# Kernel tuning notes

Hardware: AMD Instinct MI355X
Metric: run time of the kernel (lower is better)

The kernel has to match this reference:

```python
import jax, jax.numpy as jnp
import numpy as np

B, T, C, H = 4, 2048, 1024, 16
D = C // H  # head dim = 64


def setup_inputs() -> dict:
    key = jax.random.key(0)
    ks = jax.random.split(key, 5)
    s = 1.0 / np.sqrt(C)
    return {
        "x": jax.random.normal(ks[0], (B, T, C), dtype=jnp.float32),
        "Wq": jax.random.normal(ks[1], (C, C), dtype=jnp.float32) * s,
        "bq": jnp.zeros((C,), dtype=jnp.float32),
        "Wk": jax.random.normal(ks[2], (C, C), dtype=jnp.float32) * s,
        "bk": jnp.zeros((C,), dtype=jnp.float32),
        "Wv": jax.random.normal(ks[3], (C, C), dtype=jnp.float32) * s,
        "bv": jnp.zeros((C,), dtype=jnp.float32),
        "Wp": jax.random.normal(ks[4], (C, C), dtype=jnp.float32) * s,
        "bp": jnp.zeros((C,), dtype=jnp.float32),
    }


def reference(x, Wq, bq, Wk, bk, Wv, bv, Wp, bp):
    Bb, Tt, Cc = x.shape
    # QKV projections (torch Linear: y = x @ W.T + b)
    q = (x @ Wq.T + bq).reshape(Bb, Tt, H, D).transpose(0, 2, 1, 3)  # [B,H,T,D]
    k = (x @ Wk.T + bk).reshape(Bb, Tt, H, D).transpose(0, 2, 1, 3)
    v = (x @ Wv.T + bv).reshape(Bb, Tt, H, D).transpose(0, 2, 1, 3)
    att = jnp.einsum("bhqd,bhkd->bhqk", q, k) / jnp.sqrt(jnp.float32(D))
    causal = jnp.tril(jnp.ones((Tt, Tt), dtype=bool))
    att = jnp.where(causal[None, None], att, -jnp.inf)
    att = jax.nn.softmax(att, axis=-1)
    y = jnp.einsum("bhqk,bhkd->bhqd", att, v)  # [B,H,T,D]
    y = y.transpose(0, 2, 1, 3).reshape(Bb, Tt, Cc)
    return y @ Wp.T + bp
```

## Files before the change

kernel.cpp:

```cpp
#include <hip/hip_runtime.h>

typedef unsigned short u16;
typedef unsigned int u32;

typedef __attribute__((ext_vector_type(4))) float f32x4;
typedef __attribute__((ext_vector_type(8))) short bf16x8;


__device__ inline u16 f2b(float f) {
  union { float f; u32 u; } x; x.f = f;
  u32 u = x.u;
  u32 r = (u + 0x7fffu + ((u >> 16) & 1u)) >> 16;
  return (u16)r;
}

__device__ inline u32 cvtpk(float lo, float hi) {
  u32 r;
  asm("v_cvt_pk_bf16_f32 %0, %1, %2" : "=v"(r) : "v"(lo), "v"(hi));
  return r;
}

__device__ inline void gload_lds16(const void* g, void* l) {
  __builtin_amdgcn_global_load_lds(
      (const __attribute__((address_space(1))) u32*)g,
      (__attribute__((address_space(3))) u32*)l, 16, 0, 0);
}


__global__ __launch_bounds__(256) void cvt_all(const float* __restrict__ x,
                                               const float* __restrict__ w0,
                                               const float* __restrict__ w1,
                                               const float* __restrict__ w2,
                                               const float* __restrict__ w3,
                                               u16* __restrict__ xs,
                                               u16* __restrict__ wsz,
                                               u16* __restrict__ wp) {
  int b = blockIdx.x, t = threadIdx.x;
  const float* src;
  char* dst;
  if (b < 5632) {
    int g = b * 256 + t;
    int row;
    if (b < 4096) {
      row = g >> 7;
      src = x + (size_t)row * 1024;
      dst = (char*)xs;
    } else {
      g -= 1048576;
      row = g >> 7;
      src = (row < 1024) ? w0 + (size_t)row * 1024
           : (row < 2048) ? w1 + (size_t)(row - 1024) * 1024
                          : w2 + (size_t)(row - 2048) * 1024;
      dst = (char*)wsz;
    }
    int c = g & 127;
    int kt = c >> 3, cc = (c & 7) ^ (row & 7);
    float4 lo = *(const float4*)(src + c * 8);
    float4 hi = *(const float4*)(src + c * 8 + 4);
    union { u16 s[8]; uint4 v; } o;
    o.s[0] = f2b(lo.x); o.s[1] = f2b(lo.y); o.s[2] = f2b(lo.z); o.s[3] = f2b(lo.w);
    o.s[4] = f2b(hi.x); o.s[5] = f2b(hi.y); o.s[6] = f2b(hi.z); o.s[7] = f2b(hi.w);
    *(uint4*)(dst + (size_t)(row >> 8) * 524288 + kt * 32768 +
              (row & 255) * 128 + cc * 16) = o.v;
  } else {
    int g = (b - 5632) * 256 + t;
    float4 lo = *(const float4*)(w3 + (size_t)g * 8);
    float4 hi = *(const float4*)(w3 + (size_t)g * 8 + 4);
    union { u16 s[8]; uint4 v; } o;
    o.s[0] = f2b(lo.x); o.s[1] = f2b(lo.y); o.s[2] = f2b(lo.z); o.s[3] = f2b(lo.w);
    o.s[4] = f2b(hi.x); o.s[5] = f2b(hi.y); o.s[6] = f2b(hi.z); o.s[7] = f2b(hi.w);
    *(uint4*)((char*)wp + (size_t)g * 16) = o.v;
  }
}


__global__ __launch_bounds__(512) void gemm_qkv(const u16* __restrict__ Aswz,
                                                const u16* __restrict__ Wswz,
                                                const float* __restrict__ bq,
                                                const float* __restrict__ bk,
                                                const float* __restrict__ bv,
                                                u16* __restrict__ outQ,
                                                u16* __restrict__ outK,
                                                u16* __restrict__ outVt,
                                                float qscale) {
  __shared__ u16 sA[2][16384];
  __shared__ u16 sB[2][16384];

  const int t = threadIdx.x;
  const int lane = t & 63;
  const int w = t >> 6;
  const int wm = w >> 2, wn = w & 3;
  const int lr = lane & 15, lg = lane >> 4;

  int bid = blockIdx.y * 12 + blockIdx.x;
  int swz = (bid & 7) * 48 + (bid >> 3);
  const int mBase = (swz / 12) * 256;
  const int nBase = (swz % 12) * 256;
  const int mode = nBase >> 10;

  const char* Ap = (const char*)Aswz + (size_t)(mBase >> 8) * 524288;
  const char* Bp = (const char*)Wswz + (size_t)(nBase >> 8) * 524288;

  f32x4 acc[8][4];
#pragma unroll
  for (int i = 0; i < 8; ++i)
#pragma unroll
    for (int j = 0; j < 4; ++j) acc[i][j] = (f32x4){0.f, 0.f, 0.f, 0.f};

  auto stage8 = [&](int buf, int kt) {
    const char* As = Ap + (size_t)kt * 32768;
    const char* Bs = Bp + (size_t)kt * 32768;
    char* Ad = (char*)&sA[buf][0];
    char* Bd = (char*)&sB[buf][0];
#pragma unroll
    for (int l = 0; l < 4; ++l) {
      int off = (l * 512 + t) * 16;
      gload_lds16(As + off, Ad + off);
      gload_lds16(Bs + off, Bd + off);
    }
  };

  stage8(0, 0);
  asm volatile("s_waitcnt vmcnt(0)" ::: "memory");
  __builtin_amdgcn_s_barrier();

  for (int kt = 0; kt < 16; ++kt) {
    const int cur = kt & 1;
    const char* Ab = (const char*)&sA[cur][0];
    const char* Bb = (const char*)&sB[cur][0];

#pragma unroll
    for (int p = 0; p < 4; ++p) {
      if (p == 0 && kt + 1 < 16) stage8(cur ^ 1, kt + 1);

      const int qi = p >> 1, qj = p & 1;
      bf16x8 af[4][2], bf[2][2];
#pragma unroll
      for (int ii = 0; ii < 4; ++ii) {
        int row = wm * 128 + (qi * 4 + ii) * 16 + lr;
#pragma unroll
        for (int kk = 0; kk < 2; ++kk)
          af[ii][kk] = *(const bf16x8*)(Ab + row * 128 +
                                        ((kk * 64 + lg * 16) ^ ((row & 7) << 4)));
      }
#pragma unroll
      for (int jj = 0; jj < 2; ++jj) {
        int rn = wn * 64 + (qj * 2 + jj) * 16 + lr;
#pragma unroll
        for (int kk = 0; kk < 2; ++kk)
          bf[jj][kk] = *(const bf16x8*)(Bb + rn * 128 +
                                        ((kk * 64 + lg * 16) ^ ((rn & 7) << 4)));
      }

      __builtin_amdgcn_s_barrier();

      __builtin_amdgcn_s_setprio(1);
#pragma unroll
      for (int ii = 0; ii < 4; ++ii)
#pragma unroll
        for (int jj = 0; jj < 2; ++jj)
#pragma unroll
          for (int kk = 0; kk < 2; ++kk)
            acc[qi * 4 + ii][qj * 2 + jj] =
                __builtin_amdgcn_mfma_f32_16x16x32_bf16(
                    af[ii][kk], bf[jj][kk], acc[qi * 4 + ii][qj * 2 + jj],
                    0, 0, 0);
      __builtin_amdgcn_s_setprio(0);

      if (p == 3) asm volatile("s_waitcnt vmcnt(0)" ::: "memory");
      __builtin_amdgcn_s_barrier();
    }
  }

#pragma unroll
  for (int i = 0; i < 8; ++i) {
    int row = mBase + wm * 128 + i * 16 + lg * 4;
    int b_ = row >> 11, tp = row & 2047;
#pragma unroll
    for (int j = 0; j < 4; ++j) {
      int col = nBase + wn * 64 + j * 16 + lr;
      int ncol = col & 1023;
      int h = ncol >> 6, dd = ncol & 63;
      size_t bhOff = (size_t)(b_ * 16 + h) * 262144;
      if (mode == 2) {
        float bv_ = bv[ncol];
        ushort4 o;
        o.x = f2b(acc[i][j][0] + bv_);
        o.y = f2b(acc[i][j][1] + bv_);
        o.z = f2b(acc[i][j][2] + bv_);
        o.w = f2b(acc[i][j][3] + bv_);
        *(ushort4*)((char*)outVt + bhOff + (tp >> 6) * 8192 + dd * 128 +
                    ((((tp & 63) >> 3) << 4) ^ ((dd & 7) << 4)) +
                    (tp & 7) * 2) = o;
      } else if (mode == 0) {
        float bv_ = bq[ncol];
#pragma unroll
        for (int r = 0; r < 4; ++r)
          outQ[(((size_t)(b_ * 16 + h) * 2048) + tp + r) * 64 + dd] =
              f2b((acc[i][j][r] + bv_) * qscale);
      } else {
        float bv_ = bk[ncol];
#pragma unroll
        for (int r = 0; r < 4; ++r) {
          int tt = tp + r;
          *(u16*)((char*)outK + bhOff + (tt >> 6) * 8192 + (tt & 63) * 128 +
                  (((dd >> 3) << 4) ^ ((tt & 7) << 4)) + (dd & 7) * 2) =
              f2b(acc[i][j][r] + bv_);
        }
      }
    }
  }
}


__global__ __launch_bounds__(256) void gemm_proj(const u16* __restrict__ A,
                                                 const u16* __restrict__ W,
                                                 const float* __restrict__ bias,
                                                 float* __restrict__ outF) {
  __shared__ u16 sA[8192];
  __shared__ u16 sB[8192];

  const int K = 1024, N = 1024;
  const int t = threadIdx.x;
  const int lane = t & 63;
  const int w = t >> 6;
  const int wr = w >> 1, wc = w & 1;
  const int lr = lane & 15, lg = lane >> 4;

  int bid = blockIdx.y * 8 + blockIdx.x;
  int swz = (bid & 7) * 64 + (bid >> 3);
  const int mBase = (swz >> 3) * 128;
  const int nBase = (swz & 7) * 128;

  f32x4 zero = {0.f, 0.f, 0.f, 0.f};
  f32x4 acc[4][4];
#pragma unroll
  for (int i = 0; i < 4; ++i)
#pragma unroll
    for (int j = 0; j < 4; ++j) acc[i][j] = zero;

  const int rA = t >> 2;
  const int cA = (t & 3) * 8;

  for (int k0 = 0; k0 < K; k0 += 64) {
#pragma unroll
    for (int hh = 0; hh < 2; ++hh)
#pragma unroll
      for (int i = 0; i < 2; ++i) {
        gload_lds16(A + (size_t)(mBase + i * 64 + rA) * K + k0 + hh * 32 + cA,
                    &sA[hh * 4096 + i * 2048 + t * 8]);
        gload_lds16(W + (size_t)(nBase + i * 64 + rA) * K + k0 + hh * 32 + cA,
                    &sB[hh * 4096 + i * 2048 + t * 8]);
      }
    __syncthreads();

#pragma unroll
    for (int hh = 0; hh < 2; ++hh) {
      bf16x8 af[4], bf[4];
#pragma unroll
      for (int i = 0; i < 4; ++i)
        af[i] = *(const bf16x8*)&sA[hh * 4096 +
                                    (wr * 64 + i * 16 + lr) * 32 + lg * 8];
#pragma unroll
      for (int j = 0; j < 4; ++j)
        bf[j] = *(const bf16x8*)&sB[hh * 4096 +
                                    (wc * 64 + j * 16 + lr) * 32 + lg * 8];

#pragma unroll
      for (int i = 0; i < 4; ++i)
#pragma unroll
        for (int j = 0; j < 4; ++j)
          acc[i][j] = __builtin_amdgcn_mfma_f32_16x16x32_bf16(af[i], bf[j],
                                                              acc[i][j], 0, 0, 0);
    }
    __syncthreads();
  }

#pragma unroll
  for (int i = 0; i < 4; ++i) {
    int row = mBase + wr * 64 + i * 16 + lg * 4;
#pragma unroll
    for (int j = 0; j < 4; ++j) {
      int col = nBase + wc * 64 + j * 16 + lr;
      float bv = bias[col];
#pragma unroll
      for (int r = 0; r < 4; ++r)
        outF[(size_t)(row + r) * N + col] = acc[i][j][r] + bv;
    }
  }
}


__global__ __launch_bounds__(512) void attn_fwd(const u16* __restrict__ qg,
                                                const u16* __restrict__ kswz,
                                                const u16* __restrict__ vswz,
                                                u16* __restrict__ yg) {
  __shared__ u16 sK[2][64 * 64];
  __shared__ u16 sVt[2][64 * 64];

  const int t = threadIdx.x;
  const int lane = t & 63;
  const int w = t >> 6;
  const int lr = lane & 15, lg = lane >> 4;
  const int xk = (lr & 7) << 4;

  int bid0 = blockIdx.y * 8 + blockIdx.x;
  int swzb = (bid0 & 7) * 64 + (bid0 >> 3);
  const int bh = swzb >> 3;
  const int pair = swzb & 7;

  const char* kgb = (const char*)kswz + (size_t)bh * 262144;
  const char* vgb = (const char*)vswz + (size_t)bh * 262144;
  const u16* qb = qg + (size_t)bh * 131072;

  gload_lds16(kgb + t * 16, (char*)&sK[0][0] + t * 16);
  gload_lds16(vgb + t * 16, (char*)&sVt[0][0] + t * 16);

  f32x4 zero = {0.f, 0.f, 0.f, 0.f};
  const int b = bh >> 4, h = bh & 15;
  int tc = 0;

  for (int half = 0; half < 2; ++half) {
    const int qt = half ? pair : 15 - pair;
    const int nkt = 2 * qt + 2;
    const int wq0 = qt * 128 + w * 16;
    const int qrow = wq0 + lr;

    bf16x8 qf[2];
#pragma unroll
    for (int kk = 0; kk < 2; ++kk)
      qf[kk] = *(const bf16x8*)(qb + (size_t)qrow * 64 + kk * 32 + lg * 8);

    f32x4 accO[4];
#pragma unroll
    for (int n = 0; n < 4; ++n) accO[n] = zero;
    float lrun = 0.f;

    for (int kt = 0; kt < nkt; ++kt, ++tc) {
      const int cur = tc & 1;
      __syncthreads();

      int nextT = (kt + 1 < nkt) ? kt + 1 : (half == 0 ? 0 : -1);
      if (nextT >= 0) {
        gload_lds16(kgb + nextT * 8192 + t * 16,
                    (char*)&sK[cur ^ 1][0] + t * 16);
        gload_lds16(vgb + nextT * 8192 + t * 16,
                    (char*)&sVt[cur ^ 1][0] + t * 16);
      }

      if (kt * 64 > wq0 + 15) continue;

      const char* kb_ = (const char*)&sK[cur][0];
      const char* vb_ = (const char*)&sVt[cur][0];

      f32x4 s[4];
      __builtin_amdgcn_s_setprio(1);
#pragma unroll
      for (int n = 0; n < 4; ++n) {
        f32x4 a = zero;
#pragma unroll
        for (int kk = 0; kk < 2; ++kk) {
          bf16x8 kf = *(const bf16x8*)(kb_ + (n * 16 + lr) * 128 +
                                       ((kk * 64 + lg * 16) ^ xk));
          a = __builtin_amdgcn_mfma_f32_16x16x32_bf16(kf, qf[kk], a, 0, 0, 0);
        }
        s[n] = a;
      }
      __builtin_amdgcn_s_setprio(0);

      if (kt * 64 + 63 > wq0) {
#pragma unroll
        for (int n = 0; n < 4; ++n) {
          int key0 = kt * 64 + n * 16 + lg * 4;
#pragma unroll
          for (int r = 0; r < 4; ++r)
            s[n][r] = (key0 + r <= qrow) ? s[n][r] : -1e30f;
        }
      }

      u32 pk[4][2];
#pragma unroll
      for (int n = 0; n < 4; ++n) {
        float p0 = exp2f(s[n][0] - 12.f);
        float p1 = exp2f(s[n][1] - 12.f);
        float p2 = exp2f(s[n][2] - 12.f);
        float p3 = exp2f(s[n][3] - 12.f);
        lrun += (p0 + p1) + (p2 + p3);
        pk[n][0] = cvtpk(p0, p1);
        pk[n][1] = cvtpk(p2, p3);
      }

      const bool hi = (lg >> 1) & 1;
#pragma unroll
      for (int kk = 0; kk < 2; ++kk) {
        u32 g[4];
#pragma unroll
        for (int r = 0; r < 4; ++r) {
          const int rh = r >> 1, rl = r & 1;
          u32 give = ((lg & 1) ^ rh) ? pk[2 * kk + 1][rl] : pk[2 * kk][rl];
          int srcLane = ((lg & 1) * 2 + ((lg >> 1) ^ rh)) * 16 + lr;
          g[r] = (u32)__shfl((int)give, srcLane);
        }
        union { u32 u[4]; bf16x8 v; } pu;
        pu.u[0] = hi ? g[2] : g[0];
        pu.u[1] = hi ? g[3] : g[1];
        pu.u[2] = hi ? g[0] : g[2];
        pu.u[3] = hi ? g[1] : g[3];
        bf16x8 pf = pu.v;
        __builtin_amdgcn_s_setprio(1);
#pragma unroll
        for (int n = 0; n < 4; ++n) {
          bf16x8 vf = *(const bf16x8*)(vb_ + (n * 16 + lr) * 128 +
                                       ((kk * 64 + lg * 16) ^ xk));
          accO[n] = __builtin_amdgcn_mfma_f32_16x16x32_bf16(pf, vf, accO[n], 0, 0, 0);
        }
        __builtin_amdgcn_s_setprio(0);
      }
    }

    lrun += __shfl_xor(lrun, 16);
    lrun += __shfl_xor(lrun, 32);

#pragma unroll
    for (int r = 0; r < 4; ++r) {
      float linv = 1.f / __shfl(lrun, lg * 4 + r);
      int trow = qt * 128 + w * 16 + lg * 4 + r;
      size_t rowOff = ((size_t)b * 2048 + trow) * 1024 + h * 64;
#pragma unroll
      for (int n = 0; n < 4; ++n)
        yg[rowOff + n * 16 + lr] = f2b(accO[n][r] * linv);
    }
  }
}


extern "C" void kernel_launch(void* const* d_in, const int* in_sizes, int n_in,
                              void* d_out, int out_size, void* d_ws, size_t ws_size,
                              hipStream_t stream) {
  const float* x  = (const float*)d_in[0];
  const float* Wq = (const float*)d_in[1];
  const float* bq = (const float*)d_in[2];
  const float* Wk = (const float*)d_in[3];
  const float* bk = (const float*)d_in[4];
  const float* Wv = (const float*)d_in[5];
  const float* bv = (const float*)d_in[6];
  const float* Wp = (const float*)d_in[7];
  const float* bp = (const float*)d_in[8];
  float* out = (float*)d_out;

  char* ws = (char*)d_ws;
  u16* xb  = (u16*)(ws);
  u16* wqb = (u16*)(ws + (16u << 20));
  u16* wpb = (u16*)(ws + (22u << 20));
  u16* qb  = (u16*)(ws + (24u << 20));
  u16* kb  = (u16*)(ws + (40u << 20));
  u16* vtb = (u16*)(ws + (56u << 20));
  u16* yb  = (u16*)(ws + (72u << 20));

  const float SCL = 0.18033688011112042f;

  cvt_all<<<6144, 256, 0, stream>>>(x, Wq, Wk, Wv, Wp, xb, wqb, wpb);

  gemm_qkv<<<dim3(12, 32), 512, 0, stream>>>(xb, wqb, bq, bk, bv,
                                             qb, kb, vtb, SCL);

  attn_fwd<<<dim3(8, 64), 512, 0, stream>>>(qb, kb, vtb, yb);

  gemm_proj<<<dim3(8, 64), 256, 0, stream>>>(yb, wpb, bp, out);
}
```

Baseline: 209.5 us.

## Retile QKV GEMM to 256x128 tiles with triple-buffered LDS pipeline

The QKV projection GEMM moves from 256x256 tiles (384 blocks) to 256x128 tiles (768 blocks), with a 4x2 wave layout in which each wave owns a 64x64 sub-tile. The double-buffered stage with per-phase barriers becomes a three-stage LDS ring that prefetches two k-steps ahead and waits with a partial vmcnt. This gives better load balance across CUs and fewer barriers per k-step, at the cost of lower reuse of A per block and more A traffic from global memory.

```diff
diff --git a/kernel.cpp b/kernel.cpp
--- a/kernel.cpp
+++ b/kernel.cpp
@@ -83,98 +83,90 @@
                                                 u16* __restrict__ outK,
                                                 u16* __restrict__ outVt,
                                                 float qscale) {
-  __shared__ u16 sA[2][16384];
-  __shared__ u16 sB[2][16384];
+  __shared__ u16 lds[3][24576];
 
   const int t = threadIdx.x;
   const int lane = t & 63;
   const int w = t >> 6;
-  const int wm = w >> 2, wn = w & 3;
+  const int wm = w >> 1, wn = w & 1;
   const int lr = lane & 15, lg = lane >> 4;
 
-  int bid = blockIdx.y * 12 + blockIdx.x;
-  int swz = (bid & 7) * 48 + (bid >> 3);
-  const int mBase = (swz / 12) * 256;
-  const int nBase = (swz % 12) * 256;
+  int bid = blockIdx.y * 24 + blockIdx.x;
+  int swz = (bid & 7) * 96 + (bid >> 3);
+  const int mBase = (swz / 24) * 256;
+  const int nBase = (swz % 24) * 128;
   const int mode = nBase >> 10;
+  const int noff = nBase & 255;
 
   const char* Ap = (const char*)Aswz + (size_t)(mBase >> 8) * 524288;
-  const char* Bp = (const char*)Wswz + (size_t)(nBase >> 8) * 524288;
-
-  f32x4 acc[8][4];
-#pragma unroll
-  for (int i = 0; i < 8; ++i)
+  const char* Bp = (const char*)Wswz + (size_t)(nBase >> 8) * 524288 +
+                   noff * 128;
+
+  f32x4 acc[4][4];
+#pragma unroll
+  for (int i = 0; i < 4; ++i)
 #pragma unroll
     for (int j = 0; j < 4; ++j) acc[i][j] = (f32x4){0.f, 0.f, 0.f, 0.f};
 
-  auto stage8 = [&](int buf, int kt) {
-    const char* As = Ap + (size_t)kt * 32768;
-    const char* Bs = Bp + (size_t)kt * 32768;
-    char* Ad = (char*)&sA[buf][0];
-    char* Bd = (char*)&sB[buf][0];
-#pragma unroll
-    for (int l = 0; l < 4; ++l) {
-      int off = (l * 512 + t) * 16;
-      gload_lds16(As + off, Ad + off);
-      gload_lds16(Bs + off, Bd + off);
-    }
+  auto stage = [&](int buf, int kt2) {
+    const char* As = Ap + (size_t)kt2 * 32768;
+    const char* Bs = Bp + (size_t)kt2 * 32768;
+    char* Ad = (char*)&lds[buf][0];
+    char* Bd = (char*)&lds[buf][16384];
+#pragma unroll
+    for (int l = 0; l < 4; ++l)
+      gload_lds16(As + (l * 512 + t) * 16, Ad + (l * 512 + t) * 16);
+#pragma unroll
+    for (int l = 0; l < 2; ++l)
+      gload_lds16(Bs + (l * 512 + t) * 16, Bd + (l * 512 + t) * 16);
   };
 
-  stage8(0, 0);
-  asm volatile("s_waitcnt vmcnt(0)" ::: "memory");
-  __builtin_amdgcn_s_barrier();
+  stage(0, 0);
+  stage(1, 1);
 
   for (int kt = 0; kt < 16; ++kt) {
-    const int cur = kt & 1;
-    const char* Ab = (const char*)&sA[cur][0];
-    const char* Bb = (const char*)&sB[cur][0];
-
-#pragma unroll
-    for (int p = 0; p < 4; ++p) {
-      if (p == 0 && kt + 1 < 16) stage8(cur ^ 1, kt + 1);
-
-      const int qi = p >> 1, qj = p & 1;
-      bf16x8 af[4][2], bf[2][2];
-#pragma unroll
-      for (int ii = 0; ii < 4; ++ii) {
-        int row = wm * 128 + (qi * 4 + ii) * 16 + lr;
+    if (kt < 15) asm volatile("s_waitcnt vmcnt(6)" ::: "memory");
+    else         asm volatile("s_waitcnt vmcnt(0)" ::: "memory");
+    __builtin_amdgcn_s_barrier();
+    if (kt + 2 < 16) stage((kt + 2) % 3, kt + 2);
+
+    const int cb = kt % 3;
+    const char* Ab = (const char*)&lds[cb][0];
+    const char* Bb = (const char*)&lds[cb][16384];
+
+    bf16x8 af[4][2], bf[4][2];
+#pragma unroll
+    for (int i = 0; i < 4; ++i) {
+      int row = wm * 64 + i * 16 + lr;
+#pragma unroll
+      for (int kk = 0; kk < 2; ++kk)
+        af[i][kk] = *(const bf16x8*)(Ab + row * 128 +
+                                     ((kk * 64 + lg * 16) ^ ((row & 7) << 4)));
+    }
+#pragma unroll
+    for (int j = 0; j < 4; ++j) {
+      int rn = wn * 64 + j * 16 + lr;
+#pragma unroll
+      for (int kk = 0; kk < 2; ++kk)
+        bf[j][kk] = *(const bf16x8*)(Bb + rn * 128 +
+                                     ((kk * 64 + lg * 16) ^ ((rn & 7) << 4)));
+    }
+
+    __builtin_amdgcn_s_setprio(1);
+#pragma unroll
+    for (int i = 0; i < 4; ++i)
+#pragma unroll
+      for (int j = 0; j < 4; ++j)
 #pragma unroll
         for (int kk = 0; kk < 2; ++kk)
-          af[ii][kk] = *(const bf16x8*)(Ab + row * 128 +
-                                        ((kk * 64 + lg * 16) ^ ((row & 7) << 4)));
-      }
-#pragma unroll
-      for (int jj = 0; jj < 2; ++jj) {
-        int rn = wn * 64 + (qj * 2 + jj) * 16 + lr;
-#pragma unroll
-        for (int kk = 0; kk < 2; ++kk)
-          bf[jj][kk] = *(const bf16x8*)(Bb + rn * 128 +
-                                        ((kk * 64 + lg * 16) ^ ((rn & 7) << 4)));
-      }
-
-      __builtin_amdgcn_s_barrier();
-
-      __builtin_amdgcn_s_setprio(1);
-#pragma unroll
-      for (int ii = 0; ii < 4; ++ii)
-#pragma unroll
-        for (int jj = 0; jj < 2; ++jj)
-#pragma unroll
-          for (int kk = 0; kk < 2; ++kk)
-            acc[qi * 4 + ii][qj * 2 + jj] =
-                __builtin_amdgcn_mfma_f32_16x16x32_bf16(
-                    af[ii][kk], bf[jj][kk], acc[qi * 4 + ii][qj * 2 + jj],
-                    0, 0, 0);
-      __builtin_amdgcn_s_setprio(0);
-
-      if (p == 3) asm volatile("s_waitcnt vmcnt(0)" ::: "memory");
-      __builtin_amdgcn_s_barrier();
-    }
-  }
-
-#pragma unroll
-  for (int i = 0; i < 8; ++i) {
-    int row = mBase + wm * 128 + i * 16 + lg * 4;
+          acc[i][j] = __builtin_amdgcn_mfma_f32_16x16x32_bf16(
+              af[i][kk], bf[j][kk], acc[i][j], 0, 0, 0);
+    __builtin_amdgcn_s_setprio(0);
+  }
+
+#pragma unroll
+  for (int i = 0; i < 4; ++i) {
+    int row = mBase + wm * 64 + i * 16 + lg * 4;
     int b_ = row >> 11, tp = row & 2047;
 #pragma unroll
     for (int j = 0; j < 4; ++j) {
@@ -461,7 +453,7 @@
 
   cvt_all<<<6144, 256, 0, stream>>>(x, Wq, Wk, Wv, Wp, xb, wqb, wpb);
 
-  gemm_qkv<<<dim3(12, 32), 512, 0, stream>>>(xb, wqb, bq, bk, bv,
+  gemm_qkv<<<dim3(24, 32), 512, 0, stream>>>(xb, wqb, bq, bk, bv,
                                              qb, kb, vtb, SCL);
 
   attn_fwd<<<dim3(8, 64), 512, 0, stream>>>(qb, kb, vtb, yb);
```

Result: faster. 184.0 us (-12.2%).
